# Kernel optimization log

Hardware: AMD Instinct MI355X
Metric: run time of the kernel (lower is better)

## Reference

```python
import jax, jax.numpy as jnp
import numpy as np

B, IN, H = 8192, 1024, 1024

def _ln(x, g, b, eps=1e-5):
    mu = jnp.mean(x, axis=-1, keepdims=True)
    var = jnp.mean(jnp.square(x - mu), axis=-1, keepdims=True)
    return (x - mu) * jax.lax.rsqrt(var + eps) * g + b

def setup_inputs() -> dict:
    key = jax.random.key(0)
    ks = jax.random.split(key, 8)
    s_h = 1.0 / np.sqrt(H)
    s_i = 1.0 / np.sqrt(IN)
    inp = {
        'x': jax.random.normal(ks[0], (B, IN), jnp.float32),
        'h': jax.random.normal(ks[1], (B, H), jnp.float32),
        'W_r': jax.random.uniform(ks[2], (H, H), jnp.float32, -s_h, s_h),
        'U_r': jax.random.uniform(ks[3], (H, IN), jnp.float32, -s_i, s_i),
        'W_u': jax.random.uniform(ks[4], (H, H), jnp.float32, -s_h, s_h),
        'U_u': jax.random.uniform(ks[5], (H, IN), jnp.float32, -s_i, s_i),
        'W_c': jax.random.uniform(ks[6], (H, H), jnp.float32, -s_h, s_h),
        'U_c': jax.random.uniform(ks[7], (H, IN), jnp.float32, -s_i, s_i),
        # LayerNorm params: rows = [r_hidden, r_input, u_hidden, u_input, c_hidden, c_input]
        'ln_gamma': 0.1 * jnp.ones((6, H), jnp.float32),
        'ln_beta': jnp.zeros((6, H), jnp.float32),
    }
    return inp

def reference(x, h, W_r, U_r, W_u, U_u, W_c, U_c, ln_gamma, ln_beta):
    g, b = ln_gamma, ln_beta
    # nn.Linear(bias=False): y = x @ W.T
    r = jax.nn.sigmoid(_ln(h @ W_r.T, g[0], b[0]) + _ln(x @ U_r.T, g[1], b[1]))
    u = jax.nn.sigmoid(_ln(h @ W_u.T, g[2], b[2]) + _ln(x @ U_u.T, g[3], b[3]))
    c = jnp.tanh(_ln((h * r) @ W_c.T, g[4], b[4]) + _ln(x @ U_c.T, g[5], b[5]))
    return (1.0 - u) * h + u * c
```

## Files before the change

kernel.cpp:

```cpp
#include <hip/hip_runtime.h>
#include <cstdint>
#include <cstddef>

typedef unsigned short u16;
typedef __attribute__((ext_vector_type(8))) short bf16x8;
typedef __attribute__((ext_vector_type(4))) float f32x4;

__device__ inline float bf2f(u16 u) { return __uint_as_float(((unsigned)u) << 16); }
__device__ inline u16 f2bf(float f) {
  unsigned u = __float_as_uint(f);
  u += 0x7fffu + ((u >> 16) & 1u);
  return (u16)(u >> 16);
}

__device__ inline void async16(const u16* g, u16* l) {
  __builtin_amdgcn_global_load_lds(
      (const __attribute__((address_space(1))) void*)g,
      (__attribute__((address_space(3))) void*)l, 16, 0, 0);
}

__device__ inline void unpack8(uint4 q, float* o) {
  o[0] = bf2f((u16)(q.x & 0xffffu)); o[1] = bf2f((u16)(q.x >> 16));
  o[2] = bf2f((u16)(q.y & 0xffffu)); o[3] = bf2f((u16)(q.y >> 16));
  o[4] = bf2f((u16)(q.z & 0xffffu)); o[5] = bf2f((u16)(q.z >> 16));
  o[6] = bf2f((u16)(q.w & 0xffffu)); o[7] = bf2f((u16)(q.w >> 16));
}

__device__ inline uint4 pack8(const float* v) {
  uint4 q;
  q.x = (unsigned)f2bf(v[0]) | ((unsigned)f2bf(v[1]) << 16);
  q.y = (unsigned)f2bf(v[2]) | ((unsigned)f2bf(v[3]) << 16);
  q.z = (unsigned)f2bf(v[4]) | ((unsigned)f2bf(v[5]) << 16);
  q.w = (unsigned)f2bf(v[6]) | ((unsigned)f2bf(v[7]) << 16);
  return q;
}

__device__ inline float fast_sigmoid(float z) {
  return 1.0f / (1.0f + exp2f(-1.4426950408889634f * z));
}
__device__ inline float fast_tanh(float z) {
  return 1.0f - 2.0f / (1.0f + exp2f(2.8853900817779268f * z));
}

struct ConvAll { const float* src[8]; u16* dst[8]; };

__global__ __launch_bounds__(256) void convert_all(ConvAll a) {
  const int b = blockIdx.x;
  int which, off;
  if (b < 8192)        { which = 0; off = b; }
  else if (b < 16384)  { which = 1; off = b - 8192; }
  else { const int t = b - 16384; which = 2 + (t >> 10); off = t & 1023; }
  const float* __restrict__ s = a.src[which];
  u16* __restrict__ d = a.dst[which];
  const int i = (off * 256 + threadIdx.x) * 4;
  float4 v = *(const float4*)(s + i);
  uint2 o;
  o.x = (unsigned)f2bf(v.x) | ((unsigned)f2bf(v.y) << 16);
  o.y = (unsigned)f2bf(v.z) | ((unsigned)f2bf(v.w) << 16);
  *(uint2*)(d + i) = o;
}

struct GemmArgs { const u16* A[5]; const u16* Bw[5]; u16* Y[5]; };

__global__ __launch_bounds__(256) void gemm_bt128(GemmArgs args) {
  const int p = blockIdx.x;
  const int xcd = p & 7;
  const int s = p >> 3;
  int gate, r, col;
  if (s < 128) {
    const int pr = s >> 4;
    const int cc = s & 15;
    gate = (cc >> 3) * 2;
    col = cc & 7;
    r = pr * 8 + xcd;
  } else {
    const int s2 = s - 128;
    const int pr = s2 / 24;
    const int cc = s2 - pr * 24;
    const int gi = cc >> 3;
    gate = (gi == 0) ? 1 : ((gi == 1) ? 3 : 4);
    col = cc & 7;
    r = pr * 8 + xcd;
  }

  const u16* __restrict__ A  = args.A[gate];
  const u16* __restrict__ Bw = args.Bw[gate];
  u16* __restrict__ Y = args.Y[gate];

  __shared__ __attribute__((aligned(16))) u16 As[128 * 64];
  __shared__ __attribute__((aligned(16))) u16 Bs[128 * 64];

  const int tid  = threadIdx.x;
  const int lane = tid & 63;
  const int w    = tid >> 6;
  const int wm   = w >> 1;
  const int wn   = w & 1;

  const int rowBlk = r * 128;
  const int colBlk = col * 128;

  const int srow = lane >> 3;
  const int scol = ((lane & 7) ^ srow) * 8;
  const u16* gA[4]; const u16* gB[4]; u16* lA[4]; u16* lB[4];
#pragma unroll
  for (int i = 0; i < 4; i++) {
    const int rr = w * 32 + i * 8;
    gA[i] = A  + (size_t)(rowBlk + rr + srow) * 1024 + scol;
    gB[i] = Bw + (size_t)(colBlk + rr + srow) * 1024 + scol;
    lA[i] = &As[rr * 64];
    lB[i] = &Bs[rr * 64];
  }

  const int swz = (((lane >> 4) ^ (lane & 7)) << 3);
  const int fa = (wm * 64 + (lane & 15)) * 64 + swz;
  const int fb = (wn * 64 + (lane & 15)) * 64 + swz;

  f32x4 acc[4][4] = {};

  for (int k0 = 0; k0 < 1024; k0 += 64) {
#pragma unroll
    for (int i = 0; i < 4; i++) {
      async16(gA[i] + k0, lA[i]);
      async16(gB[i] + k0, lB[i]);
    }
    __syncthreads();
#pragma unroll
    for (int kk = 0; kk < 2; kk++) {
      const int kx = kk << 5;
      bf16x8 af[4], bfr[4];
#pragma unroll
      for (int t = 0; t < 4; t++) {
        af[t]  = *(const bf16x8*)&As[(fa + t * 1024) ^ kx];
        bfr[t] = *(const bf16x8*)&Bs[(fb + t * 1024) ^ kx];
      }
#pragma unroll
      for (int tm = 0; tm < 4; tm++)
#pragma unroll
        for (int tn = 0; tn < 4; tn++)
          acc[tm][tn] = __builtin_amdgcn_mfma_f32_16x16x32_bf16(af[tm], bfr[tn], acc[tm][tn], 0, 0, 0);
    }
    __syncthreads();
  }

  const int rBase = rowBlk + wm * 64 + (lane >> 4) * 4;
  const int cBase = colBlk + wn * 64 + (lane & 15);
#pragma unroll
  for (int tm = 0; tm < 4; tm++) {
#pragma unroll
    for (int i = 0; i < 4; i++) {
      const size_t rr = (size_t)(rBase + tm * 16 + i);
#pragma unroll
      for (int tn = 0; tn < 4; tn++)
        Y[rr * 1024 + cBase + tn * 16] = f2bf(acc[tm][tn][i]);
    }
  }
}

__global__ __launch_bounds__(256) void gemm_hr(const u16* __restrict__ A,
                                               const u16* __restrict__ Bw,
                                               u16* __restrict__ Y) {
  const int p = blockIdx.x;
  const int xcd = p & 7;
  const int s = p >> 3;
  const int col = s & 7;
  const int r = (s >> 3) * 8 + xcd;

  __shared__ __attribute__((aligned(16))) u16 As[64 * 64];
  __shared__ __attribute__((aligned(16))) u16 Bs[128 * 64];

  const int tid  = threadIdx.x;
  const int lane = tid & 63;
  const int w    = tid >> 6;
  const int wm   = w >> 1;
  const int wn   = w & 1;

  const int rowBlk = r * 64;
  const int colBlk = col * 128;

  const int srow = lane >> 3;
  const int scol = ((lane & 7) ^ srow) * 8;
  const u16* gA[2]; u16* lA[2];
  const u16* gB[4]; u16* lB[4];
#pragma unroll
  for (int i = 0; i < 2; i++) {
    const int rr = w * 16 + i * 8;
    gA[i] = A + (size_t)(rowBlk + rr + srow) * 1024 + scol;
    lA[i] = &As[rr * 64];
  }
#pragma unroll
  for (int i = 0; i < 4; i++) {
    const int rr = w * 32 + i * 8;
    gB[i] = Bw + (size_t)(colBlk + rr + srow) * 1024 + scol;
    lB[i] = &Bs[rr * 64];
  }

  const int swz = (((lane >> 4) ^ (lane & 7)) << 3);
  const int fa = (wm * 32 + (lane & 15)) * 64 + swz;
  const int fb = (wn * 64 + (lane & 15)) * 64 + swz;

  f32x4 acc[2][4] = {};

  for (int k0 = 0; k0 < 1024; k0 += 64) {
#pragma unroll
    for (int i = 0; i < 2; i++) async16(gA[i] + k0, lA[i]);
#pragma unroll
    for (int i = 0; i < 4; i++) async16(gB[i] + k0, lB[i]);
    __syncthreads();
#pragma unroll
    for (int kk = 0; kk < 2; kk++) {
      const int kx = kk << 5;
      bf16x8 af[2], bfr[4];
#pragma unroll
      for (int t = 0; t < 2; t++) af[t]  = *(const bf16x8*)&As[(fa + t * 1024) ^ kx];
#pragma unroll
      for (int t = 0; t < 4; t++) bfr[t] = *(const bf16x8*)&Bs[(fb + t * 1024) ^ kx];
#pragma unroll
      for (int tm = 0; tm < 2; tm++)
#pragma unroll
        for (int tn = 0; tn < 4; tn++)
          acc[tm][tn] = __builtin_amdgcn_mfma_f32_16x16x32_bf16(af[tm], bfr[tn], acc[tm][tn], 0, 0, 0);
    }
    __syncthreads();
  }

  const int rBase = rowBlk + wm * 32 + (lane >> 4) * 4;
  const int cBase = colBlk + wn * 64 + (lane & 15);
#pragma unroll
  for (int tm = 0; tm < 2; tm++) {
#pragma unroll
    for (int i = 0; i < 4; i++) {
      const size_t rr = (size_t)(rBase + tm * 16 + i);
#pragma unroll
      for (int tn = 0; tn < 4; tn++)
        Y[rr * 1024 + cBase + tn * 16] = f2bf(acc[tm][tn][i]);
    }
  }
}

__global__ __launch_bounds__(256) void rgate_kernel(
    const u16* __restrict__ Yrh, const u16* __restrict__ Yrx,
    const u16* __restrict__ hb, const float* __restrict__ gamma,
    const float* __restrict__ beta, u16* __restrict__ hrb) {
  const int row  = blockIdx.x * 4 + (threadIdx.x >> 6);
  const int lane = threadIdx.x & 63;
  const size_t rb = (size_t)row * 1024;

  uint4 qa[2], qb[2], qh[2];
  qa[0] = *(const uint4*)(Yrh + rb + lane * 8);
  qa[1] = *(const uint4*)(Yrh + rb + 512 + lane * 8);
  qb[0] = *(const uint4*)(Yrx + rb + lane * 8);
  qb[1] = *(const uint4*)(Yrx + rb + 512 + lane * 8);
  qh[0] = *(const uint4*)(hb  + rb + lane * 8);
  qh[1] = *(const uint4*)(hb  + rb + 512 + lane * 8);

  float s0 = 0.f, s0q = 0.f, s1 = 0.f, s1q = 0.f;
  float tmp[8];
#pragma unroll
  for (int c = 0; c < 2; c++) {
    unpack8(qa[c], tmp);
#pragma unroll
    for (int j = 0; j < 8; j++) { s0 += tmp[j]; s0q += tmp[j] * tmp[j]; }
    unpack8(qb[c], tmp);
#pragma unroll
    for (int j = 0; j < 8; j++) { s1 += tmp[j]; s1q += tmp[j] * tmp[j]; }
  }
#pragma unroll
  for (int off = 1; off < 64; off <<= 1) {
    s0 += __shfl_xor(s0, off, 64);  s0q += __shfl_xor(s0q, off, 64);
    s1 += __shfl_xor(s1, off, 64);  s1q += __shfl_xor(s1q, off, 64);
  }

  const float inv = 1.0f / 1024.0f;
  const float mu0 = s0 * inv, rs0 = rsqrtf(s0q * inv - mu0 * mu0 + 1e-5f);
  const float mu1 = s1 * inv, rs1 = rsqrtf(s1q * inv - mu1 * mu1 + 1e-5f);

#pragma unroll
  for (int c = 0; c < 2; c++) {
    const int cb = c * 512 + lane * 8;
    float va[8], vb[8], vh[8], o[8];
    unpack8(qa[c], va); unpack8(qb[c], vb); unpack8(qh[c], vh);
#pragma unroll
    for (int j = 0; j < 8; j++) {
      const float ln0 = (va[j] - mu0) * rs0 * gamma[cb + j] + beta[cb + j];
      const float ln1 = (vb[j] - mu1) * rs1 * gamma[1024 + cb + j] + beta[1024 + cb + j];
      const float rg = fast_sigmoid(ln0 + ln1);
      o[j] = vh[j] * rg;
    }
    *(uint4*)(hrb + rb + cb) = pack8(o);
  }
}

__global__ __launch_bounds__(256) void final_fuse(
    const u16* __restrict__ Yuh, const u16* __restrict__ Yux,
    const u16* __restrict__ Ych, const u16* __restrict__ Ycx,
    const float* __restrict__ h, const float* __restrict__ gamma,
    const float* __restrict__ beta, float* __restrict__ out) {
  const int row  = blockIdx.x * 4 + (threadIdx.x >> 6);
  const int lane = threadIdx.x & 63;
  const size_t rb = (size_t)row * 1024;

  uint4 q0[2], q1[2], q2[2], q3[2];
  float4 hf[4];
#pragma unroll
  for (int c = 0; c < 2; c++) {
    const int cb = c * 512 + lane * 8;
    q0[c] = *(const uint4*)(Yuh + rb + cb);
    q1[c] = *(const uint4*)(Yux + rb + cb);
    q2[c] = *(const uint4*)(Ych + rb + cb);
    q3[c] = *(const uint4*)(Ycx + rb + cb);
    hf[c * 2]     = *(const float4*)(h + rb + cb);
    hf[c * 2 + 1] = *(const float4*)(h + rb + cb + 4);
  }

  float s[8] = {0.f, 0.f, 0.f, 0.f, 0.f, 0.f, 0.f, 0.f};
  float tmp[8];
#pragma unroll
  for (int c = 0; c < 2; c++) {
    unpack8(q0[c], tmp);
#pragma unroll
    for (int j = 0; j < 8; j++) { s[0] += tmp[j]; s[1] += tmp[j] * tmp[j]; }
    unpack8(q1[c], tmp);
#pragma unroll
    for (int j = 0; j < 8; j++) { s[2] += tmp[j]; s[3] += tmp[j] * tmp[j]; }
    unpack8(q2[c], tmp);
#pragma unroll
    for (int j = 0; j < 8; j++) { s[4] += tmp[j]; s[5] += tmp[j] * tmp[j]; }
    unpack8(q3[c], tmp);
#pragma unroll
    for (int j = 0; j < 8; j++) { s[6] += tmp[j]; s[7] += tmp[j] * tmp[j]; }
  }
#pragma unroll
  for (int off = 1; off < 64; off <<= 1) {
#pragma unroll
    for (int q = 0; q < 8; q++) s[q] += __shfl_xor(s[q], off, 64);
  }

  const float inv = 1.0f / 1024.0f;
  const float mu0 = s[0] * inv, rs0 = rsqrtf(s[1] * inv - mu0 * mu0 + 1e-5f);
  const float mu1 = s[2] * inv, rs1 = rsqrtf(s[3] * inv - mu1 * mu1 + 1e-5f);
  const float mu2 = s[4] * inv, rs2 = rsqrtf(s[5] * inv - mu2 * mu2 + 1e-5f);
  const float mu3 = s[6] * inv, rs3 = rsqrtf(s[7] * inv - mu3 * mu3 + 1e-5f);

#pragma unroll
  for (int c = 0; c < 2; c++) {
    const int cb = c * 512 + lane * 8;
    float v0[8], v1[8], v2[8], v3[8];
    unpack8(q0[c], v0); unpack8(q1[c], v1); unpack8(q2[c], v2); unpack8(q3[c], v3);
    const float* hv = (const float*)&hf[c * 2];
    float o[8];
#pragma unroll
    for (int j = 0; j < 8; j++) {
      const int cc = cb + j;
      const float ln2 = (v0[j] - mu0) * rs0 * gamma[2 * 1024 + cc] + beta[2 * 1024 + cc];
      const float ln3 = (v1[j] - mu1) * rs1 * gamma[3 * 1024 + cc] + beta[3 * 1024 + cc];
      const float ln4 = (v2[j] - mu2) * rs2 * gamma[4 * 1024 + cc] + beta[4 * 1024 + cc];
      const float ln5 = (v3[j] - mu3) * rs3 * gamma[5 * 1024 + cc] + beta[5 * 1024 + cc];
      const float u  = fast_sigmoid(ln2 + ln3);
      const float cg = fast_tanh(ln4 + ln5);
      o[j] = (1.0f - u) * hv[j] + u * cg;
    }
    *(float4*)(out + rb + cb)     = *(float4*)&o[0];
    *(float4*)(out + rb + cb + 4) = *(float4*)&o[4];
  }
}

extern "C" void kernel_launch(void* const* d_in, const int* in_sizes, int n_in,
                              void* d_out, int out_size, void* d_ws, size_t ws_size,
                              hipStream_t stream) {
  const float* x  = (const float*)d_in[0];
  const float* h  = (const float*)d_in[1];
  const float* Ws[6] = {(const float*)d_in[2], (const float*)d_in[3],
                        (const float*)d_in[4], (const float*)d_in[5],
                        (const float*)d_in[6], (const float*)d_in[7]};
  const float* gamma = (const float*)d_in[8];
  const float* beta  = (const float*)d_in[9];
  float* out = (float*)d_out;

  char* ws = (char*)d_ws;
  const size_t SZ_ACT = (size_t)8192 * 1024 * 2;
  const size_t SZ_W   = (size_t)1024 * 1024 * 2;

  u16* xb = (u16*)(ws);
  u16* hb = (u16*)(ws + SZ_ACT);
  u16* wb[6];
  for (int i = 0; i < 6; i++) wb[i] = (u16*)(ws + 2 * SZ_ACT + i * SZ_W);
  char* ybase = ws + 2 * SZ_ACT + 6 * SZ_W;
  u16* Y0 = (u16*)(ybase);
  u16* Y1 = (u16*)(ybase + SZ_ACT);
  u16* Y2 = (u16*)(ybase + 2 * SZ_ACT);
  u16* Y3 = (u16*)(ybase + 3 * SZ_ACT);
  u16* Y5 = (u16*)(ybase + 4 * SZ_ACT);

  ConvAll ca = {};
  ca.src[0] = x; ca.dst[0] = xb;
  ca.src[1] = h; ca.dst[1] = hb;
  for (int i = 0; i < 6; i++) { ca.src[2 + i] = Ws[i]; ca.dst[2 + i] = wb[i]; }
  convert_all<<<16384 + 6 * 1024, 256, 0, stream>>>(ca);

  GemmArgs g = {};
  g.A[0] = hb; g.Bw[0] = wb[0]; g.Y[0] = Y0;
  g.A[1] = xb; g.Bw[1] = wb[1]; g.Y[1] = Y1;
  g.A[2] = hb; g.Bw[2] = wb[2]; g.Y[2] = Y2;
  g.A[3] = xb; g.Bw[3] = wb[3]; g.Y[3] = Y3;
  g.A[4] = xb; g.Bw[4] = wb[5]; g.Y[4] = Y5;
  gemm_bt128<<<2560, 256, 0, stream>>>(g);

  rgate_kernel<<<2048, 256, 0, stream>>>(Y0, Y1, hb, gamma, beta, Y1);

  gemm_hr<<<1024, 256, 0, stream>>>(Y1, wb[4], Y0);

  final_fuse<<<2048, 256, 0, stream>>>(Y2, Y3, Y0, Y5, h, gamma, beta, out);
}
```

Measured before the change: 296.3 us.

## Rebalance GEMM launches: batch only r-gate GEMMs first, fold hr GEMM into second batch

The first GEMM launch now computes only the two r-gate products (h·W_r, x·U_r) so the r-gate kernel can start sooner. The remaining u/c gate GEMMs are moved after the r-gate and batched together with the (h*r)·W_c GEMM into one launch of 2048 blocks using the 128x128 tile kernel. This drops the separate 64-row tile hr kernel and gives both launches evenly sized, full-wave grids. The cost is that the 2048-block launch must wait for the r-gate kernel before starting.

```diff
diff --git a/kernel.cpp b/kernel.cpp
--- a/kernel.cpp
+++ b/kernel.cpp
@@ -60,28 +60,18 @@
   *(uint2*)(d + i) = o;
 }
 
-struct GemmArgs { const u16* A[5]; const u16* Bw[5]; u16* Y[5]; };
-
-__global__ __launch_bounds__(256) void gemm_bt128(GemmArgs args) {
+struct Gemm4 { const u16* A[4]; const u16* Bw[4]; u16* Y[4]; };
+
+template <int NG_LOG2>
+__global__ __launch_bounds__(256) void gemm_batch(Gemm4 args) {
   const int p = blockIdx.x;
   const int xcd = p & 7;
   const int s = p >> 3;
-  int gate, r, col;
-  if (s < 128) {
-    const int pr = s >> 4;
-    const int cc = s & 15;
-    gate = (cc >> 3) * 2;
-    col = cc & 7;
-    r = pr * 8 + xcd;
-  } else {
-    const int s2 = s - 128;
-    const int pr = s2 / 24;
-    const int cc = s2 - pr * 24;
-    const int gi = cc >> 3;
-    gate = (gi == 0) ? 1 : ((gi == 1) ? 3 : 4);
-    col = cc & 7;
-    r = pr * 8 + xcd;
-  }
+  const int pr = s >> (3 + NG_LOG2);
+  const int cc = s & ((8 << NG_LOG2) - 1);
+  const int gate = cc >> 3;
+  const int col  = cc & 7;
+  const int r = pr * 8 + xcd;
 
   const u16* __restrict__ A  = args.A[gate];
   const u16* __restrict__ Bw = args.Bw[gate];
@@ -146,87 +136,6 @@
   const int cBase = colBlk + wn * 64 + (lane & 15);
 #pragma unroll
   for (int tm = 0; tm < 4; tm++) {
-#pragma unroll
-    for (int i = 0; i < 4; i++) {
-      const size_t rr = (size_t)(rBase + tm * 16 + i);
-#pragma unroll
-      for (int tn = 0; tn < 4; tn++)
-        Y[rr * 1024 + cBase + tn * 16] = f2bf(acc[tm][tn][i]);
-    }
-  }
-}
-
-__global__ __launch_bounds__(256) void gemm_hr(const u16* __restrict__ A,
-                                               const u16* __restrict__ Bw,
-                                               u16* __restrict__ Y) {
-  const int p = blockIdx.x;
-  const int xcd = p & 7;
-  const int s = p >> 3;
-  const int col = s & 7;
-  const int r = (s >> 3) * 8 + xcd;
-
-  __shared__ __attribute__((aligned(16))) u16 As[64 * 64];
-  __shared__ __attribute__((aligned(16))) u16 Bs[128 * 64];
-
-  const int tid  = threadIdx.x;
-  const int lane = tid & 63;
-  const int w    = tid >> 6;
-  const int wm   = w >> 1;
-  const int wn   = w & 1;
-
-  const int rowBlk = r * 64;
-  const int colBlk = col * 128;
-
-  const int srow = lane >> 3;
-  const int scol = ((lane & 7) ^ srow) * 8;
-  const u16* gA[2]; u16* lA[2];
-  const u16* gB[4]; u16* lB[4];
-#pragma unroll
-  for (int i = 0; i < 2; i++) {
-    const int rr = w * 16 + i * 8;
-    gA[i] = A + (size_t)(rowBlk + rr + srow) * 1024 + scol;
-    lA[i] = &As[rr * 64];
-  }
-#pragma unroll
-  for (int i = 0; i < 4; i++) {
-    const int rr = w * 32 + i * 8;
-    gB[i] = Bw + (size_t)(colBlk + rr + srow) * 1024 + scol;
-    lB[i] = &Bs[rr * 64];
-  }
-
-  const int swz = (((lane >> 4) ^ (lane & 7)) << 3);
-  const int fa = (wm * 32 + (lane & 15)) * 64 + swz;
-  const int fb = (wn * 64 + (lane & 15)) * 64 + swz;
-
-  f32x4 acc[2][4] = {};
-
-  for (int k0 = 0; k0 < 1024; k0 += 64) {
-#pragma unroll
-    for (int i = 0; i < 2; i++) async16(gA[i] + k0, lA[i]);
-#pragma unroll
-    for (int i = 0; i < 4; i++) async16(gB[i] + k0, lB[i]);
-    __syncthreads();
-#pragma unroll
-    for (int kk = 0; kk < 2; kk++) {
-      const int kx = kk << 5;
-      bf16x8 af[2], bfr[4];
-#pragma unroll
-      for (int t = 0; t < 2; t++) af[t]  = *(const bf16x8*)&As[(fa + t * 1024) ^ kx];
-#pragma unroll
-      for (int t = 0; t < 4; t++) bfr[t] = *(const bf16x8*)&Bs[(fb + t * 1024) ^ kx];
-#pragma unroll
-      for (int tm = 0; tm < 2; tm++)
-#pragma unroll
-        for (int tn = 0; tn < 4; tn++)
-          acc[tm][tn] = __builtin_amdgcn_mfma_f32_16x16x32_bf16(af[tm], bfr[tn], acc[tm][tn], 0, 0, 0);
-    }
-    __syncthreads();
-  }
-
-  const int rBase = rowBlk + wm * 32 + (lane >> 4) * 4;
-  const int cBase = colBlk + wn * 64 + (lane & 15);
-#pragma unroll
-  for (int tm = 0; tm < 2; tm++) {
 #pragma unroll
     for (int i = 0; i < 4; i++) {
       const size_t rr = (size_t)(rBase + tm * 16 + i);
@@ -397,17 +306,19 @@
   for (int i = 0; i < 6; i++) { ca.src[2 + i] = Ws[i]; ca.dst[2 + i] = wb[i]; }
   convert_all<<<16384 + 6 * 1024, 256, 0, stream>>>(ca);
 
-  GemmArgs g = {};
-  g.A[0] = hb; g.Bw[0] = wb[0]; g.Y[0] = Y0;
-  g.A[1] = xb; g.Bw[1] = wb[1]; g.Y[1] = Y1;
-  g.A[2] = hb; g.Bw[2] = wb[2]; g.Y[2] = Y2;
-  g.A[3] = xb; g.Bw[3] = wb[3]; g.Y[3] = Y3;
-  g.A[4] = xb; g.Bw[4] = wb[5]; g.Y[4] = Y5;
-  gemm_bt128<<<2560, 256, 0, stream>>>(g);
+  Gemm4 ga = {};
+  ga.A[0] = hb; ga.Bw[0] = wb[0]; ga.Y[0] = Y0;
+  ga.A[1] = xb; ga.Bw[1] = wb[1]; ga.Y[1] = Y1;
+  gemm_batch<1><<<1024, 256, 0, stream>>>(ga);
 
   rgate_kernel<<<2048, 256, 0, stream>>>(Y0, Y1, hb, gamma, beta, Y1);
 
-  gemm_hr<<<1024, 256, 0, stream>>>(Y1, wb[4], Y0);
+  Gemm4 gb = {};
+  gb.A[0] = xb; gb.Bw[0] = wb[3]; gb.Y[0] = Y3;
+  gb.A[1] = xb; gb.Bw[1] = wb[5]; gb.Y[1] = Y5;
+  gb.A[2] = hb; gb.Bw[2] = wb[2]; gb.Y[2] = Y2;
+  gb.A[3] = Y1; gb.Bw[3] = wb[4]; gb.Y[3] = Y0;
+  gemm_batch<2><<<2048, 256, 0, stream>>>(gb);
 
   final_fuse<<<2048, 256, 0, stream>>>(Y2, Y3, Y0, Y5, h, gamma, beta, out);
 }
```

Result: no change. 299.2 us (+1.0%).
